# Kernel tuning notes

Hardware: AMD Instinct MI355X
Metric: run time of the kernel (lower is better)

Reference implementation:

```python
import jax, jax.numpy as jnp
import numpy as np

B = 2_097_152
S_IN = 13
H = 16
N_HIDDEN = 30  # layer_num - 2


def _uniform(key, shape, fan_in):
    bound = 1.0 / np.sqrt(fan_in)
    return jax.random.uniform(key, shape, jnp.float32, -bound, bound)


def setup_inputs() -> dict:
    key = jax.random.key(0)
    ks = jax.random.split(key, 8)
    x = jax.random.normal(ks[0], (B, S_IN), jnp.float32)
    W_in = _uniform(ks[1], (H, S_IN), S_IN)
    b_in = _uniform(ks[2], (H,), S_IN)
    W_h = _uniform(ks[3], (N_HIDDEN, H, H), H)
    b_h = _uniform(ks[4], (N_HIDDEN, H), H)
    W_out = _uniform(ks[5], (1, H), H)
    b_out = _uniform(ks[6], (1,), H)
    return {"x": x, "W_in": W_in, "b_in": b_in, "W_h": W_h,
            "b_h": b_h, "W_out": W_out, "b_out": b_out}


def reference(x, W_in, b_in, W_h, b_h, W_out, b_out):
    # in_layer + ReLU: [B, S_IN] -> [B, H]
    h = jax.nn.relu(x @ W_in.T + b_in)

    # 30 hidden Linear+ReLU layers, scanned over stacked weights
    def step(h, wb):
        W, b = wb  # W: [H, H], b: [H]
        return jax.nn.relu(h @ W.T + b), None

    h, _ = jax.lax.scan(step, h, (W_h, b_h))

    # out1: [B, H] -> [B, 1], then squeeze -> [B]
    y = h @ W_out.T + b_out
    return y.squeeze(-1)
```

## Files before the change

kernel.cpp:

```cpp
#include <hip/hip_runtime.h>
#include <stdint.h>


typedef __attribute__((ext_vector_type(4))) _Float16 half4v;
typedef __attribute__((ext_vector_type(2))) _Float16 h2;
typedef __attribute__((ext_vector_type(4))) float float4v;

#define S_IN 13
#define H 16
#define NL 32
#define TPB 1024
#define WPB 16
#define T 4
#define NBLOCKS 512
#define STRIDE (NBLOCKS * WPB * T)

#define XS_BASE 4608
#define LDS_DW (XS_BASE + WPB * 832 + 4)

__device__ __forceinline__ unsigned pkh(float a, float b) {
    return __builtin_bit_cast(unsigned, __builtin_amdgcn_cvt_pkrtz(a, b));
}

__device__ __forceinline__ half4v pack4h(float v0, float v1, float v2, float v3) {
    int2 p;
    p.x = (int)pkh(v0, v1);
    p.y = (int)pkh(v2, v3);
    return __builtin_bit_cast(half4v, p);
}

__device__ __forceinline__ half4v relu_pack4h(const float4v& d) {
    const h2 z = {(_Float16)0.f, (_Float16)0.f};
    h2 lo = __builtin_bit_cast(h2, pkh(d[0], d[1]));
    h2 hi = __builtin_bit_cast(h2, pkh(d[2], d[3]));
    lo = __builtin_elementwise_max(lo, z);
    hi = __builtin_elementwise_max(hi, z);
    int2 p;
    p.x = __builtin_bit_cast(int, lo);
    p.y = __builtin_bit_cast(int, hi);
    return __builtin_bit_cast(half4v, p);
}

__global__ __launch_bounds__(TPB, 8)
void mlp_kernel(const float* __restrict__ x,
                const float* __restrict__ W_in, const float* __restrict__ b_in,
                const float* __restrict__ W_h,  const float* __restrict__ b_h,
                const float* __restrict__ W_out,const float* __restrict__ b_out,
                float* __restrict__ out, int tiles)
{
    __shared__ unsigned lds[LDS_DW];
    const int tid = threadIdx.x;

    for (int s = tid; s < NL * 64; s += TPB) {
        const int L = s >> 6, ln = s & 63, m = ln & 15, gg = ln >> 4;
        float v[4];
#pragma unroll
        for (int i = 0; i < 4; ++i) {
            const int k = 4 * gg + i;
            if (L == 0)       v[i] = (k < S_IN) ? W_in[m * S_IN + k] : 0.f;
            else if (L <= 30) v[i] = W_h[(L - 1) * H * H + m * H + k];
            else              v[i] = (m == 0) ? W_out[k] : 0.f;
        }
        lds[s * 2]     = pkh(v[0], v[1]);
        lds[s * 2 + 1] = pkh(v[2], v[3]);
    }
    for (int s = tid; s < NL * H; s += TPB) {
        const int L = s >> 4, m = s & 15;
        float bv;
        if (L == 0)       bv = b_in[m];
        else if (L <= 30) bv = b_h[(L - 1) * H + m];
        else              bv = (m == 0) ? b_out[0] : 0.f;
        lds[4096 + s] = __float_as_uint(bv);
    }
    if (tid < 4) lds[XS_BASE + WPB * 832 + tid] = 0;
    __syncthreads();

    const half4v* lA = (const half4v*)lds;
    const float4v* lB = (const float4v*)(lds + 4096);

    const int lane = tid & 63;
    const int wv   = tid >> 6;
    const int g    = lane >> 4;
    const int col  = lane & 15;
    const int k0   = 4 * g;
    const int col13k = col * 13 + k0;

    unsigned* xs = lds + XS_BASE + wv * 832;

    const int wave_id = blockIdx.x * WPB + wv;
    int tb = wave_id * T;
    if (tb >= tiles) return;

    float* op = out + (size_t)tb * 16 + lane;

    const float* xp = x + (size_t)tb * 208;
    float4v r0 = *(const float4v*)(xp + lane * 4);
    float4v r1 = *(const float4v*)(xp + 256 + lane * 4);
    float4v r2 = *(const float4v*)(xp + 512 + lane * 4);
    float    r3 = xp[768 + lane];

    for (; tb < tiles; tb += STRIDE) {
        *(float4v*)(xs + lane * 4)       = r0;
        *(float4v*)(xs + 256 + lane * 4) = r1;
        *(float4v*)(xs + 512 + lane * 4) = r2;
        xs[768 + lane] = __float_as_uint(r3);

        const int tbn = tb + STRIDE;
        if (tbn < tiles) {
            xp = x + (size_t)tbn * 208;
            r0 = *(const float4v*)(xp + lane * 4);
            r1 = *(const float4v*)(xp + 256 + lane * 4);
            r2 = *(const float4v*)(xp + 512 + lane * 4);
            r3 = xp[768 + lane];
        }

        half4v bf[T];
#pragma unroll
        for (int t = 0; t < T; ++t) {
            const unsigned* p = xs + t * 208 + col13k;
            bf[t] = pack4h(__uint_as_float(p[0]), __uint_as_float(p[1]),
                           __uint_as_float(p[2]), __uint_as_float(p[3]));
        }

        half4v aC = lA[lane];
        half4v aN = lA[64 + lane];
        float4v cC = lB[g];
        float4v cN = lB[4 + g];
#pragma unroll
        for (int L = 0; L < NL - 1; ++L) {
            half4v aN2;
            float4v cN2;
            if (L + 2 < NL) {
                aN2 = lA[(L + 2) * 64 + lane];
                cN2 = lB[(L + 2) * 4 + g];
            }
            float4v d[T];
#pragma unroll
            for (int t = 0; t < T; ++t)
                d[t] = __builtin_amdgcn_mfma_f32_16x16x16f16(aC, bf[t], cC, 0, 0, 0);
#pragma unroll
            for (int t = 0; t < T; ++t)
                bf[t] = relu_pack4h(d[t]);
            aC = aN; aN = aN2;
            cC = cN; cN = cN2;
        }

#pragma unroll
        for (int t = 0; t < T; ++t) {
            float4v d = __builtin_amdgcn_mfma_f32_16x16x16f16(aC, bf[t], cC, 0, 0, 0);
            if (lane < 16) op[t * 16] = d[0];
        }
        op += (size_t)STRIDE * 16;
    }
}

extern "C" void kernel_launch(void* const* d_in, const int* in_sizes, int n_in,
                              void* d_out, int out_size, void* d_ws, size_t ws_size,
                              hipStream_t stream) {
    const float* x     = (const float*)d_in[0];
    const float* W_in  = (const float*)d_in[1];
    const float* b_in  = (const float*)d_in[2];
    const float* W_h   = (const float*)d_in[3];
    const float* b_h   = (const float*)d_in[4];
    const float* W_out = (const float*)d_in[5];
    const float* b_out = (const float*)d_in[6];
    float* out = (float*)d_out;

    const int tiles = out_size / 16;
    int blocks = (tiles + WPB * T - 1) / (WPB * T);
    if (blocks > NBLOCKS) blocks = NBLOCKS;
    mlp_kernel<<<blocks, TPB, 0, stream>>>(x, W_in, b_in, W_h, b_h, W_out, b_out,
                                           out, tiles);
}
```

Before: 192.7 us.

## Load MFMA input fragments directly from global memory and double tiles per wave

Drops the LDS staging buffer for x. Each lane now does an unaligned 16-byte global load of its own 4 input features, with an edge-lane fix that avoids reading past the row, and builds its fp16 B fragment in registers. Tiles per wave go from 4 to 8, which gives more independent MFMA chains to hide latency. The cross-iteration prefetch of the next x chunk is removed, so load latency is now covered only by the other waves and the larger T, and register pressure rises.

```diff
diff --git a/kernel.cpp b/kernel.cpp
--- a/kernel.cpp
+++ b/kernel.cpp
@@ -11,12 +11,11 @@
 #define NL 32
 #define TPB 1024
 #define WPB 16
-#define T 4
+#define T 8
 #define NBLOCKS 512
 #define STRIDE (NBLOCKS * WPB * T)
 
-#define XS_BASE 4608
-#define LDS_DW (XS_BASE + WPB * 832 + 4)
+#define LDS_DW 4608
 
 __device__ __forceinline__ unsigned pkh(float a, float b) {
     return __builtin_bit_cast(unsigned, __builtin_amdgcn_cvt_pkrtz(a, b));
@@ -39,6 +38,12 @@
     p.x = __builtin_bit_cast(int, lo);
     p.y = __builtin_bit_cast(int, hi);
     return __builtin_bit_cast(half4v, p);
+}
+
+__device__ __forceinline__ float4v ld4u(const float* p) {
+    float4v r;
+    __builtin_memcpy(&r, p, 16);
+    return r;
 }
 
 __global__ __launch_bounds__(TPB, 8)
@@ -72,7 +77,6 @@
         else              bv = (m == 0) ? b_out[0] : 0.f;
         lds[4096 + s] = __float_as_uint(bv);
     }
-    if (tid < 4) lds[XS_BASE + WPB * 832 + tid] = 0;
     __syncthreads();
 
     const half4v* lA = (const half4v*)lds;
@@ -82,10 +86,8 @@
     const int wv   = tid >> 6;
     const int g    = lane >> 4;
     const int col  = lane & 15;
-    const int k0   = 4 * g;
-    const int col13k = col * 13 + k0;
-
-    unsigned* xs = lds + XS_BASE + wv * 832;
+    const bool edge = (col == 15) && (g == 3);
+    const int goff = col * 13 + 4 * g - (edge ? 3 : 0);
 
     const int wave_id = blockIdx.x * WPB + wv;
     int tb = wave_id * T;
@@ -93,33 +95,21 @@
 
     float* op = out + (size_t)tb * 16 + lane;
 
-    const float* xp = x + (size_t)tb * 208;
-    float4v r0 = *(const float4v*)(xp + lane * 4);
-    float4v r1 = *(const float4v*)(xp + 256 + lane * 4);
-    float4v r2 = *(const float4v*)(xp + 512 + lane * 4);
-    float    r3 = xp[768 + lane];
-
     for (; tb < tiles; tb += STRIDE) {
-        *(float4v*)(xs + lane * 4)       = r0;
-        *(float4v*)(xs + 256 + lane * 4) = r1;
-        *(float4v*)(xs + 512 + lane * 4) = r2;
-        xs[768 + lane] = __float_as_uint(r3);
-
-        const int tbn = tb + STRIDE;
-        if (tbn < tiles) {
-            xp = x + (size_t)tbn * 208;
-            r0 = *(const float4v*)(xp + lane * 4);
-            r1 = *(const float4v*)(xp + 256 + lane * 4);
-            r2 = *(const float4v*)(xp + 512 + lane * 4);
-            r3 = xp[768 + lane];
-        }
+        const float* xp = x + (size_t)tb * 208 + goff;
+        float4v v[T];
+#pragma unroll
+        for (int t = 0; t < T; ++t)
+            v[t] = ld4u(xp + t * 208);
 
         half4v bf[T];
 #pragma unroll
         for (int t = 0; t < T; ++t) {
-            const unsigned* p = xs + t * 208 + col13k;
-            bf[t] = pack4h(__uint_as_float(p[0]), __uint_as_float(p[1]),
-                           __uint_as_float(p[2]), __uint_as_float(p[3]));
+            const float a0 = edge ? v[t][3] : v[t][0];
+            const float a1 = edge ? 0.f : v[t][1];
+            const float a2 = edge ? 0.f : v[t][2];
+            const float a3 = edge ? 0.f : v[t][3];
+            bf[t] = pack4h(a0, a1, a2, a3);
         }
 
         half4v aC = lA[lane];
@@ -128,19 +118,17 @@
         float4v cN = lB[4 + g];
 #pragma unroll
         for (int L = 0; L < NL - 1; ++L) {
-            half4v aN2;
-            float4v cN2;
+            half4v aN2 = aN;
+            float4v cN2 = cN;
             if (L + 2 < NL) {
                 aN2 = lA[(L + 2) * 64 + lane];
                 cN2 = lB[(L + 2) * 4 + g];
             }
-            float4v d[T];
 #pragma unroll
-            for (int t = 0; t < T; ++t)
-                d[t] = __builtin_amdgcn_mfma_f32_16x16x16f16(aC, bf[t], cC, 0, 0, 0);
-#pragma unroll
-            for (int t = 0; t < T; ++t)
-                bf[t] = relu_pack4h(d[t]);
+            for (int t = 0; t < T; ++t) {
+                float4v d = __builtin_amdgcn_mfma_f32_16x16x16f16(aC, bf[t], cC, 0, 0, 0);
+                bf[t] = relu_pack4h(d);
+            }
             aC = aN; aN = aN2;
             cC = cN; cN = cN2;
         }
```

Measured after the change: 390.0 us. 102% more time.
